# Optimization experiments

Hardware: AMD Instinct MI355X
Metric: run time of the kernel (lower is better)

Reference implementation:

```python
import jax, jax.numpy as jnp
import numpy as np

N_CLASSES = 8
EPS = 1e-5


def setup_inputs() -> dict:
    key = jax.random.key(0)
    k1, k2, k3, k4 = jax.random.split(key, 4)
    B, F, L = 512, 128, 1024
    x = jax.random.normal(k1, (B, F, L), dtype=jnp.float32)
    labels = jax.random.randint(k2, (B,), 0, N_CLASSES, dtype=jnp.int32)
    weight = jax.random.normal(k3, (N_CLASSES, F), dtype=jnp.float32)
    bias = jax.random.normal(k4, (N_CLASSES, F), dtype=jnp.float32)
    return {"x": x, "labels": labels, "weight": weight, "bias": bias}


def reference(x, labels, weight, bias):
    # x: [B, F, L]; labels: [B] in [0, n_classes); weight/bias: [K, F]
    # Per-class training-mode BatchNorm1d: biased mean/var over the class's
    # (batch_subset, length) elements per feature, then per-class affine.
    B, F, L = x.shape
    mask = jax.nn.one_hot(labels, N_CLASSES, dtype=x.dtype)      # [B, K]
    cnt = jnp.maximum(mask.sum(axis=0) * L, 1.0)                  # [K] elements per class
    sum_x = jnp.einsum('bk,bfl->kf', mask, x)                     # [K, F]
    sum_x2 = jnp.einsum('bk,bfl->kf', mask, x * x)                # [K, F]
    mean = sum_x / cnt[:, None]                                   # [K, F]
    var = sum_x2 / cnt[:, None] - mean * mean                     # biased variance
    inv = jax.lax.rsqrt(var + EPS)                                # [K, F]
    scale = (inv * weight)[labels][:, :, None]                    # [B, F, 1]
    shift = (bias - mean * inv * weight)[labels][:, :, None]      # [B, F, 1]
    return x * scale + shift
```

## Files before the change

### kernel.cpp

```cpp
#include <hip/hip_runtime.h>
#include <hip/hip_cooperative_groups.h>

namespace cg = cooperative_groups;

#define B_DIM 512
#define F_DIM 128
#define L_DIM 1024
#define K_CLS 8
#define EPS 1e-5f
#define NROWS (B_DIM * F_DIM)
#define GRID  2048
#define CHUNK 32

typedef float vf4 __attribute__((ext_vector_type(4)));

#define ST_SQ (K_CLS * F_DIM)

__device__ __forceinline__ uint bf16r(float f) {
    uint u = __float_as_uint(f);
    return (u + 0x7FFFu + ((u >> 16) & 1u)) >> 16;
}
__device__ __forceinline__ uint pk(float a, float b) {
    return bf16r(a) | (bf16r(b) << 16);
}
__device__ __forceinline__ float unlo(uint u) { return __uint_as_float(u << 16); }
__device__ __forceinline__ float unhi(uint u) { return __uint_as_float(u & 0xFFFF0000u); }

__global__ __launch_bounds__(256, 8) void cbn_fused(const float* __restrict__ x,
                                                    const int* __restrict__ labels,
                                                    const float* __restrict__ weight,
                                                    const float* __restrict__ bias,
                                                    float* __restrict__ stats,
                                                    float* __restrict__ y) {
    const int tid  = threadIdx.x;
    const int wave = tid >> 6;
    const int lane = tid & 63;
    const int r0   = blockIdx.x * CHUNK;
    const int b0   = r0 >> 7;
    const int f0   = r0 & (F_DIM - 1);
    const int k    = labels[b0];

    __shared__ uint2 ldsb[8][256];
    __shared__ float s_sc[CHUNK], s_sh[CHUNK];
    __shared__ int   s_cnt;

    uint pA0, pA1, pA2, pA3, pA4, pA5, pA6, pA7;
    uint pB0, pB1, pB2, pB3, pB4, pB5, pB6, pB7;

    const vf4* xw = reinterpret_cast<const vf4*>(x) + (size_t)(r0 + wave * 8) * (L_DIM / 4);

#pragma unroll
    for (int i = 0; i < 8; ++i) {
        vf4 v0 = xw[i * 256 + 0 * 64 + lane];
        vf4 v1 = xw[i * 256 + 1 * 64 + lane];
        vf4 v2 = xw[i * 256 + 2 * 64 + lane];
        vf4 v3 = xw[i * 256 + 3 * 64 + lane];

        if (i == 0) {
            pA0 = pk(v0.x, v0.y); pA1 = pk(v0.z, v0.w);
            pA2 = pk(v1.x, v1.y); pA3 = pk(v1.z, v1.w);
            pA4 = pk(v2.x, v2.y); pA5 = pk(v2.z, v2.w);
            pA6 = pk(v3.x, v3.y); pA7 = pk(v3.z, v3.w);
        }
        if (i == 1) {
            pB0 = pk(v0.x, v0.y); pB1 = pk(v0.z, v0.w);
            pB2 = pk(v1.x, v1.y); pB3 = pk(v1.z, v1.w);
            pB4 = pk(v2.x, v2.y); pB5 = pk(v2.z, v2.w);
            pB6 = pk(v3.x, v3.y); pB7 = pk(v3.z, v3.w);
        }
        if (i == 2 || i == 3) {
            const int slot = wave * 2 + (i - 2);
            ldsb[slot][0 * 64 + lane] = make_uint2(pk(v0.x, v0.y), pk(v0.z, v0.w));
            ldsb[slot][1 * 64 + lane] = make_uint2(pk(v1.x, v1.y), pk(v1.z, v1.w));
            ldsb[slot][2 * 64 + lane] = make_uint2(pk(v2.x, v2.y), pk(v2.z, v2.w));
            ldsb[slot][3 * 64 + lane] = make_uint2(pk(v3.x, v3.y), pk(v3.z, v3.w));
        }

        float s  = (v0.x + v0.y + v0.z + v0.w) + (v1.x + v1.y + v1.z + v1.w)
                 + (v2.x + v2.y + v2.z + v2.w) + (v3.x + v3.y + v3.z + v3.w);
        float s2 = (v0.x*v0.x + v0.y*v0.y + v0.z*v0.z + v0.w*v0.w)
                 + (v1.x*v1.x + v1.y*v1.y + v1.z*v1.z + v1.w*v1.w)
                 + (v2.x*v2.x + v2.y*v2.y + v2.z*v2.z + v2.w*v2.w)
                 + (v3.x*v3.x + v3.y*v3.y + v3.z*v3.z + v3.w*v3.w);
#pragma unroll
        for (int m = 32; m >= 1; m >>= 1) {
            s  += __shfl_xor(s, m);
            s2 += __shfl_xor(s2, m);
        }
        if (lane == 0) {
            const int f = f0 + wave * 8 + i;
            atomicAdd(&stats[k * F_DIM + f], s);
            atomicAdd(&stats[ST_SQ + k * F_DIM + f], s2);
        }
    }
    cg::this_grid().sync();

    if (tid == 0) s_cnt = 0;
    __syncthreads();
    {
        int c = (labels[tid] == k) + (labels[tid + 256] == k);
#pragma unroll
        for (int m = 32; m >= 1; m >>= 1) c += __shfl_xor(c, m);
        if (lane == 0) atomicAdd(&s_cnt, c);
    }
    __syncthreads();
    if (tid < CHUNK) {
        const int f = f0 + tid;
        const float cnt  = fmaxf((float)s_cnt * (float)L_DIM, 1.0f);
        const float mean = stats[k * F_DIM + f] / cnt;
        const float var  = stats[ST_SQ + k * F_DIM + f] / cnt - mean * mean;
        const float inv  = rsqrtf(var + EPS);
        const float sc   = inv * weight[k * F_DIM + f];
        s_sc[tid] = sc;
        s_sh[tid] = bias[k * F_DIM + f] - mean * sc;
    }
    __syncthreads();

    vf4* yw = reinterpret_cast<vf4*>(y) + (size_t)(r0 + wave * 8) * (L_DIM / 4);

    {
        const float sc = s_sc[wave * 8 + 0];
        const float sh = s_sh[wave * 8 + 0];
        vf4 o;
        o.x = unlo(pA0)*sc+sh; o.y = unhi(pA0)*sc+sh; o.z = unlo(pA1)*sc+sh; o.w = unhi(pA1)*sc+sh;
        __builtin_nontemporal_store(o, &yw[0 * 256 + 0 * 64 + lane]);
        o.x = unlo(pA2)*sc+sh; o.y = unhi(pA2)*sc+sh; o.z = unlo(pA3)*sc+sh; o.w = unhi(pA3)*sc+sh;
        __builtin_nontemporal_store(o, &yw[0 * 256 + 1 * 64 + lane]);
        o.x = unlo(pA4)*sc+sh; o.y = unhi(pA4)*sc+sh; o.z = unlo(pA5)*sc+sh; o.w = unhi(pA5)*sc+sh;
        __builtin_nontemporal_store(o, &yw[0 * 256 + 2 * 64 + lane]);
        o.x = unlo(pA6)*sc+sh; o.y = unhi(pA6)*sc+sh; o.z = unlo(pA7)*sc+sh; o.w = unhi(pA7)*sc+sh;
        __builtin_nontemporal_store(o, &yw[0 * 256 + 3 * 64 + lane]);
    }
    {
        const float sc = s_sc[wave * 8 + 1];
        const float sh = s_sh[wave * 8 + 1];
        vf4 o;
        o.x = unlo(pB0)*sc+sh; o.y = unhi(pB0)*sc+sh; o.z = unlo(pB1)*sc+sh; o.w = unhi(pB1)*sc+sh;
        __builtin_nontemporal_store(o, &yw[1 * 256 + 0 * 64 + lane]);
        o.x = unlo(pB2)*sc+sh; o.y = unhi(pB2)*sc+sh; o.z = unlo(pB3)*sc+sh; o.w = unhi(pB3)*sc+sh;
        __builtin_nontemporal_store(o, &yw[1 * 256 + 1 * 64 + lane]);
        o.x = unlo(pB4)*sc+sh; o.y = unhi(pB4)*sc+sh; o.z = unlo(pB5)*sc+sh; o.w = unhi(pB5)*sc+sh;
        __builtin_nontemporal_store(o, &yw[1 * 256 + 2 * 64 + lane]);
        o.x = unlo(pB6)*sc+sh; o.y = unhi(pB6)*sc+sh; o.z = unlo(pB7)*sc+sh; o.w = unhi(pB7)*sc+sh;
        __builtin_nontemporal_store(o, &yw[1 * 256 + 3 * 64 + lane]);
    }
#pragma unroll
    for (int i = 2; i < 4; ++i) {
        const int slot = wave * 2 + (i - 2);
        const float sc = s_sc[wave * 8 + i];
        const float sh = s_sh[wave * 8 + i];
#pragma unroll
        for (int j = 0; j < 4; ++j) {
            uint2 u = ldsb[slot][j * 64 + lane];
            vf4 o;
            o.x = unlo(u.x) * sc + sh;
            o.y = unhi(u.x) * sc + sh;
            o.z = unlo(u.y) * sc + sh;
            o.w = unhi(u.y) * sc + sh;
            __builtin_nontemporal_store(o, &yw[i * 256 + j * 64 + lane]);
        }
    }
#pragma unroll
    for (int i = 4; i < 8; ++i) {
        const float sc = s_sc[wave * 8 + i];
        const float sh = s_sh[wave * 8 + i];
#pragma unroll
        for (int j = 0; j < 4; ++j) {
            vf4 v = xw[i * 256 + j * 64 + lane];
            vf4 o;
            o.x = v.x * sc + sh;
            o.y = v.y * sc + sh;
            o.z = v.z * sc + sh;
            o.w = v.w * sc + sh;
            __builtin_nontemporal_store(o, &yw[i * 256 + j * 64 + lane]);
        }
    }
}

#define ST_SQ_FB    NROWS
#define ST_SCALE_FB (2 * NROWS)
#define ST_SHIFT_FB (2 * NROWS + K_CLS * F_DIM)

__global__ __launch_bounds__(256) void cbn_stats_fb(const float* __restrict__ x,
                                                    float* __restrict__ st) {
    const int wave = threadIdx.x >> 6;
    const int lane = threadIdx.x & 63;
    const int row  = blockIdx.x * 4 + wave;
    const int b = row >> 7;
    const int f = row & (F_DIM - 1);
    const vf4* x4 = reinterpret_cast<const vf4*>(x) + (size_t)row * (L_DIM / 4);
    float s = 0.f, s2 = 0.f;
#pragma unroll
    for (int i = 0; i < 4; ++i) {
        vf4 v = x4[i * 64 + lane];
        s  += v.x + v.y + v.z + v.w;
        s2 += v.x * v.x + v.y * v.y + v.z * v.z + v.w * v.w;
    }
#pragma unroll
    for (int m = 32; m >= 1; m >>= 1) {
        s  += __shfl_xor(s, m);
        s2 += __shfl_xor(s2, m);
    }
    if (lane == 0) {
        st[f * B_DIM + b]            = s;
        st[ST_SQ_FB + f * B_DIM + b] = s2;
    }
}

__global__ __launch_bounds__(512) void cbn_finalize_fb(const int* __restrict__ labels,
                                                       const float* __restrict__ weight,
                                                       const float* __restrict__ bias,
                                                       float* __restrict__ st) {
    __shared__ float ssum[K_CLS], ssq[K_CLS];
    __shared__ int   cnt[K_CLS];
    const int f = blockIdx.x;
    const int b = threadIdx.x;
    if (b < K_CLS) { ssum[b] = 0.f; ssq[b] = 0.f; cnt[b] = 0; }
    __syncthreads();
    const int k = labels[b];
    atomicAdd(&ssum[k], st[f * B_DIM + b]);
    atomicAdd(&ssq[k],  st[ST_SQ_FB + f * B_DIM + b]);
    atomicAdd(&cnt[k], 1);
    __syncthreads();
    if (b < K_CLS) {
        const float c = fmaxf((float)cnt[b] * (float)L_DIM, 1.0f);
        const float mean = ssum[b] / c;
        const float var  = ssq[b] / c - mean * mean;
        const float inv  = rsqrtf(var + EPS);
        const float sc   = inv * weight[b * F_DIM + f];
        st[ST_SCALE_FB + b * F_DIM + f] = sc;
        st[ST_SHIFT_FB + b * F_DIM + f] = bias[b * F_DIM + f] - mean * sc;
    }
}

#define APPLY_ROWS 4
__global__ __launch_bounds__(256) void cbn_apply_fb(const float* __restrict__ x,
                                                    const int* __restrict__ labels,
                                                    const float* __restrict__ st,
                                                    float* __restrict__ y) {
    const int nBlocks = NROWS / APPLY_ROWS;
    const int blk = nBlocks - 1 - blockIdx.x;
    const int row0 = blk * APPLY_ROWS;
#pragma unroll
    for (int it = 0; it < APPLY_ROWS; ++it) {
        const int row = row0 + it;
        const int b = row >> 7;
        const int f = row & (F_DIM - 1);
        const int k = labels[b];
        const float sc = st[ST_SCALE_FB + k * F_DIM + f];
        const float sh = st[ST_SHIFT_FB + k * F_DIM + f];
        const size_t i4 = (size_t)row * (L_DIM / 4) + threadIdx.x;
        vf4 v = reinterpret_cast<const vf4*>(x)[i4];
        vf4 o;
        o.x = v.x * sc + sh;
        o.y = v.y * sc + sh;
        o.z = v.z * sc + sh;
        o.w = v.w * sc + sh;
        __builtin_nontemporal_store(o, &reinterpret_cast<vf4*>(y)[i4]);
    }
}

extern "C" void kernel_launch(void* const* d_in, const int* in_sizes, int n_in,
                              void* d_out, int out_size, void* d_ws, size_t ws_size,
                              hipStream_t stream) {
    const float* x      = (const float*)d_in[0];
    const int*   labels = (const int*)d_in[1];
    const float* weight = (const float*)d_in[2];
    const float* bias   = (const float*)d_in[3];
    float* y  = (float*)d_out;
    float* ws = (float*)d_ws;

    int blocksPerCU = 0;
    hipError_t qerr = hipOccupancyMaxActiveBlocksPerMultiprocessor(
        &blocksPerCU, (const void*)cbn_fused, 256, 0);
    const bool coop_ok = (qerr == hipSuccess) && (blocksPerCU * 256 >= GRID);

    if (coop_ok) {
        hipMemsetAsync(ws, 0, 2 * K_CLS * F_DIM * sizeof(float), stream);
        void* args[] = { (void*)&x, (void*)&labels, (void*)&weight, (void*)&bias,
                         (void*)&ws, (void*)&y };
        hipLaunchCooperativeKernel((const void*)cbn_fused, dim3(GRID), dim3(256),
                                   args, 0, stream);
    } else {
        cbn_stats_fb<<<NROWS / 4, 256, 0, stream>>>(x, ws);
        cbn_finalize_fb<<<F_DIM, 512, 0, stream>>>(labels, weight, bias, ws);
        cbn_apply_fb<<<NROWS / APPLY_ROWS, 256, 0, stream>>>(x, labels, ws, y);
    }
}
```

Before: 123.5 us.

## Replace cooperative grid sync with custom atomic barrier and nontemporal loads

Swaps cg::this_grid().sync() for a hand-rolled one-shot barrier: each block atomically increments a counter, the last arrival sets a release flag, and the others spin on that flag with s_sleep. The stats are then read with agent-scope atomic loads. The first half of x rows, which are cached in registers and LDS, are loaded nontemporally. The aim is to cut the overhead of the cooperative-groups grid barrier and reduce cache pollution from the cached data, at the cost of relying on co-residency and extra workspace memset.

```diff
diff --git a/kernel.cpp b/kernel.cpp
--- a/kernel.cpp
+++ b/kernel.cpp
@@ -1,7 +1,4 @@
 #include <hip/hip_runtime.h>
-#include <hip/hip_cooperative_groups.h>
-
-namespace cg = cooperative_groups;
 
 #define B_DIM 512
 #define F_DIM 128
@@ -31,6 +28,7 @@
                                                     const float* __restrict__ weight,
                                                     const float* __restrict__ bias,
                                                     float* __restrict__ stats,
+                                                    uint* __restrict__ gsync,
                                                     float* __restrict__ y) {
     const int tid  = threadIdx.x;
     const int wave = tid >> 6;
@@ -51,10 +49,18 @@
 
 #pragma unroll
     for (int i = 0; i < 8; ++i) {
-        vf4 v0 = xw[i * 256 + 0 * 64 + lane];
-        vf4 v1 = xw[i * 256 + 1 * 64 + lane];
-        vf4 v2 = xw[i * 256 + 2 * 64 + lane];
-        vf4 v3 = xw[i * 256 + 3 * 64 + lane];
+        vf4 v0, v1, v2, v3;
+        if (i < 4) {
+            v0 = __builtin_nontemporal_load(&xw[i * 256 + 0 * 64 + lane]);
+            v1 = __builtin_nontemporal_load(&xw[i * 256 + 1 * 64 + lane]);
+            v2 = __builtin_nontemporal_load(&xw[i * 256 + 2 * 64 + lane]);
+            v3 = __builtin_nontemporal_load(&xw[i * 256 + 3 * 64 + lane]);
+        } else {
+            v0 = xw[i * 256 + 0 * 64 + lane];
+            v1 = xw[i * 256 + 1 * 64 + lane];
+            v2 = xw[i * 256 + 2 * 64 + lane];
+            v3 = xw[i * 256 + 3 * 64 + lane];
+        }
 
         if (i == 0) {
             pA0 = pk(v0.x, v0.y); pA1 = pk(v0.z, v0.w);
@@ -93,7 +99,21 @@
             atomicAdd(&stats[ST_SQ + k * F_DIM + f], s2);
         }
     }
-    cg::this_grid().sync();
+
+    __syncthreads();
+    if (tid == 0) {
+        __threadfence();
+        const uint old = atomicAdd(&gsync[0], 1u);
+        if (old == (uint)GRID - 1u) {
+            __hip_atomic_store(&gsync[1], 1u, __ATOMIC_RELEASE, __HIP_MEMORY_SCOPE_AGENT);
+        } else {
+            while (__hip_atomic_load(&gsync[1], __ATOMIC_RELAXED, __HIP_MEMORY_SCOPE_AGENT) == 0u) {
+                __builtin_amdgcn_s_sleep(16);
+            }
+        }
+        __threadfence();
+    }
+    __syncthreads();
 
     if (tid == 0) s_cnt = 0;
     __syncthreads();
@@ -107,8 +127,10 @@
     if (tid < CHUNK) {
         const int f = f0 + tid;
         const float cnt  = fmaxf((float)s_cnt * (float)L_DIM, 1.0f);
-        const float mean = stats[k * F_DIM + f] / cnt;
-        const float var  = stats[ST_SQ + k * F_DIM + f] / cnt - mean * mean;
+        const float sum  = __hip_atomic_load(&stats[k * F_DIM + f], __ATOMIC_RELAXED, __HIP_MEMORY_SCOPE_AGENT);
+        const float sq   = __hip_atomic_load(&stats[ST_SQ + k * F_DIM + f], __ATOMIC_RELAXED, __HIP_MEMORY_SCOPE_AGENT);
+        const float mean = sum / cnt;
+        const float var  = sq / cnt - mean * mean;
         const float inv  = rsqrtf(var + EPS);
         const float sc   = inv * weight[k * F_DIM + f];
         s_sc[tid] = sc;
@@ -269,6 +291,7 @@
     const float* bias   = (const float*)d_in[3];
     float* y  = (float*)d_out;
     float* ws = (float*)d_ws;
+    uint*  gs = (uint*)((char*)d_ws + 2 * K_CLS * F_DIM * sizeof(float));
 
     int blocksPerCU = 0;
     hipError_t qerr = hipOccupancyMaxActiveBlocksPerMultiprocessor(
@@ -276,9 +299,9 @@
     const bool coop_ok = (qerr == hipSuccess) && (blocksPerCU * 256 >= GRID);
 
     if (coop_ok) {
-        hipMemsetAsync(ws, 0, 2 * K_CLS * F_DIM * sizeof(float), stream);
+        hipMemsetAsync(ws, 0, 2 * K_CLS * F_DIM * sizeof(float) + 2 * sizeof(uint), stream);
         void* args[] = { (void*)&x, (void*)&labels, (void*)&weight, (void*)&bias,
-                         (void*)&ws, (void*)&y };
+                         (void*)&ws, (void*)&gs, (void*)&y };
         hipLaunchCooperativeKernel((const void*)cbn_fused, dim3(GRID), dim3(256),
                                    args, 0, stream);
     } else {
```

Result: no change. 124.0 us (+0.4%).
